# Kernel optimization log

Hardware: AMD Instinct MI355X
Metric: run time of the kernel (lower is better)

Reference implementation:

```python
import jax, jax.numpy as jnp
import numpy as np

B, T, C, H = 4, 2048, 1024, 16


def setup_inputs() -> dict:
    key = jax.random.key(0)
    ks = jax.random.split(key, 8)
    s = 0.02
    return {
        "xq": jax.random.normal(ks[0], (B, T, C), jnp.float32),
        "xk": jax.random.normal(ks[1], (B, T, C), jnp.float32),
        "xv": jax.random.normal(ks[2], (B, T, C), jnp.float32),
        "Wq": jax.random.normal(ks[3], (C, C), jnp.float32) * s,
        "Wk": jax.random.normal(ks[4], (C, C), jnp.float32) * s,
        "Wv": jax.random.normal(ks[5], (C, C), jnp.float32) * s,
        "Wo": jax.random.normal(ks[6], (C, C), jnp.float32) * s,
        "bo": jnp.zeros((C,), jnp.float32),
    }


def reference(xq, xk, xv, Wq, Wk, Wv, Wo, bo):
    # torch nn.Linear: y = x @ W.T
    q = xq @ Wq.T  # (B,T,C)
    k = xk @ Wk.T
    v = xv @ Wv.T
    hd = C // H
    # (B,T,C) -> (B,H,T,hd)
    q = q.reshape(B, T, H, hd).transpose(0, 2, 1, 3)
    k = k.reshape(B, T, H, hd).transpose(0, 2, 1, 3)
    v = v.reshape(B, T, H, hd).transpose(0, 2, 1, 3)
    scale = 1.0 / jnp.sqrt(jnp.asarray(hd, q.dtype))
    att = jnp.einsum("bhqd,bhkd->bhqk", q, k) * scale  # (B,H,T,T)
    causal = jnp.tril(jnp.ones((T, T), bool))
    att = jnp.where(causal, att, jnp.asarray(-jnp.inf, att.dtype))
    att = jax.nn.softmax(att, axis=-1)
    y = jnp.einsum("bhqk,bhkd->bhqd", att, v)  # (B,H,T,hd)
    y = y.transpose(0, 2, 1, 3).reshape(B, T, C)
    return y @ Wo.T + bo
```

## Files before the change

kernel.cpp:

```cpp
#include <hip/hip_runtime.h>
#include <stdint.h>

#define B_ 4
#define T_ 2048
#define C_ 1024
#define H_ 16
#define HD 64

typedef __attribute__((ext_vector_type(8))) short bf16x8;
typedef __attribute__((ext_vector_type(4))) short bf16x4;
typedef __attribute__((ext_vector_type(4))) float v4f;
typedef __attribute__((ext_vector_type(4))) uint32_t v4u;

static __device__ __forceinline__ short f2bf(float f) {
    union { float f; uint32_t u; } v; v.f = f;
    uint32_t u = v.u;
    uint32_t r = (u + 0x7fffu + ((u >> 16) & 1u)) >> 16;
    return (short)(r & 0xffffu);
}
static __device__ __forceinline__ uint32_t pack2(float x, float y) {
    uint32_t a = __float_as_uint(x) + 0x8000u;
    uint32_t b = __float_as_uint(y) + 0x8000u;
    return __builtin_amdgcn_perm(b, a, 0x07060302u);
}
static __device__ __forceinline__ uint32_t pack2t(float x, float y) {
    return __builtin_amdgcn_perm(__float_as_uint(y), __float_as_uint(x), 0x07060302u);
}
static __device__ __forceinline__ void gload_lds16(const void* g, void* l) {
    __builtin_amdgcn_global_load_lds(
        (const __attribute__((address_space(1))) void*)g,
        (__attribute__((address_space(3))) void*)l, 16, 0, 0);
}

__global__ __launch_bounds__(256) void convx(
    const float* __restrict__ x0, const float* __restrict__ x1,
    short* __restrict__ o0, short* __restrict__ o1,
    const float* __restrict__ w0, const float* __restrict__ w1,
    const float* __restrict__ w2, const float* __restrict__ w3,
    short* __restrict__ wout)
{
    int bid = blockIdx.x;
    const float* src; short* dst; size_t id;
    if (bid < 8192) {
        src = (bid < 4096) ? x0 : x1;
        dst = (bid < 4096) ? o0 : o1;
        id = (size_t)(bid & 4095) * 256 + threadIdx.x;
    } else {
        int wb = bid - 8192;
        int wi = wb >> 9;
        src = (wi == 0) ? w0 : (wi == 1) ? w1 : (wi == 2) ? w2 : w3;
        dst = wout + (size_t)wi * (C_ * C_);
        id = (size_t)(wb & 511) * 256 + threadIdx.x;
    }
    const float* p = src + id * 8;
    v4f a0 = *(const v4f*)p, a1 = *(const v4f*)(p + 4);
    v4u dv;
    dv[0] = pack2(a0[0], a0[1]); dv[1] = pack2(a0[2], a0[3]);
    dv[2] = pack2(a1[0], a1[1]); dv[3] = pack2(a1[2], a1[3]);
    *(v4u*)&dst[id * 8] = dv;
}


__global__ __launch_bounds__(256) void proj_gemm(
    const short* __restrict__ Xq, const short* __restrict__ Xk,
    const short* __restrict__ Wb, const float* __restrict__ xv,
    short* __restrict__ Qh, short* __restrict__ Kh, short* __restrict__ Vt,
    float qscale)
{
    const int K = 1024;
    __shared__ short As[128 * 64];
    __shared__ short Bs[128 * 64];
    const int t = threadIdx.x;
    const int w = t >> 6, l = t & 63, g = l >> 4, c = l & 15;
    const int wm = w & 1, wn = w >> 1;
    const int z = blockIdx.z;
    const int m0 = (z == 2 ? blockIdx.y : blockIdx.x) * 128;
    const int n0 = (z == 2 ? blockIdx.x : blockIdx.y) * 128;
    const short* Ab = (z == 0) ? Xq : (z == 1) ? Xk : (Wb + 2 * C_ * C_);
    const short* Bb = (z == 0) ? Wb : (Wb + C_ * C_);

    const int srow = l >> 3;
    const int sch = (l & 7) ^ (l >> 3);
    const int rch = c & 7;

    v4f acc[4][4];
#pragma unroll
    for (int i = 0; i < 4; ++i)
#pragma unroll
        for (int j = 0; j < 4; ++j) acc[i][j] = (v4f){0.f, 0.f, 0.f, 0.f};

    for (int k0 = 0; k0 < K; k0 += 64) {
        __syncthreads();
#pragma unroll
        for (int i = 0; i < 4; ++i) {
            int sp = w * 4 + i;
            gload_lds16(Ab + (size_t)(m0 + sp * 8 + srow) * K + k0 + sch * 8,
                        &As[sp * 512]);
        }
        if (z < 2) {
#pragma unroll
            for (int i = 0; i < 4; ++i) {
                int sp = w * 4 + i;
                gload_lds16(Bb + (size_t)(n0 + sp * 8 + srow) * K + k0 + sch * 8,
                            &Bs[sp * 512]);
            }
        } else {
#pragma unroll
            for (int i = 0; i < 4; ++i) {
                int id = i * 256 + t;
                int rr = id >> 3, cc = id & 7;
                const float* p = xv + (size_t)(n0 + rr) * K + k0 + cc * 8;
                v4f a0 = *(const v4f*)p, a1 = *(const v4f*)(p + 4);
                v4u dv;
                dv[0] = pack2(a0[0], a0[1]); dv[1] = pack2(a0[2], a0[3]);
                dv[2] = pack2(a1[0], a1[1]); dv[3] = pack2(a1[2], a1[3]);
                *(v4u*)&Bs[rr * 64 + ((cc ^ (rr & 7)) * 8)] = dv;
            }
        }
        __syncthreads();
#pragma unroll
        for (int s = 0; s < 2; ++s) {
            const int kch = ((4 * s + g) ^ rch) * 8;
            bf16x8 af[4], bfr[4];
#pragma unroll
            for (int i = 0; i < 4; ++i)
                af[i] = *(const bf16x8*)&As[(wm * 64 + i * 16 + c) * 64 + kch];
#pragma unroll
            for (int j = 0; j < 4; ++j)
                bfr[j] = *(const bf16x8*)&Bs[(wn * 64 + j * 16 + c) * 64 + kch];
#pragma unroll
            for (int i = 0; i < 4; ++i)
#pragma unroll
                for (int j = 0; j < 4; ++j)
                    acc[i][j] = __builtin_amdgcn_mfma_f32_16x16x32_bf16(af[i], bfr[j], acc[i][j], 0, 0, 0);
        }
    }
    if (z < 2) {
        short* Out = (z == 0) ? Qh : Kh;
        const float os = (z == 0) ? qscale : 1.0f;
#pragma unroll
        for (int i = 0; i < 4; ++i)
#pragma unroll
            for (int j = 0; j < 4; ++j)
#pragma unroll
                for (int r = 0; r < 4; ++r) {
                    int m = m0 + wm * 64 + i * 16 + g * 4 + r;
                    int n = n0 + wn * 64 + j * 16 + c;
                    int b = m >> 11, tt = m & (T_ - 1);
                    int h = n >> 6, d = n & 63;
                    Out[((size_t)(b * H_ + h) * T_ + tt) * HD + d] = f2bf(acc[i][j][r] * os);
                }
    } else {
#pragma unroll
        for (int i = 0; i < 4; ++i)
#pragma unroll
            for (int j = 0; j < 4; ++j)
#pragma unroll
                for (int r = 0; r < 4; ++r) {
                    int m = m0 + wm * 64 + i * 16 + g * 4 + r;
                    int n = n0 + wn * 64 + j * 16 + c;
                    int b = n >> 11, tt = n & (T_ - 1);
                    int h = m >> 6, d = m & 63;
                    Vt[((size_t)(b * H_ + h) * HD + d) * T_ + tt] = f2bf(acc[i][j][r]);
                }
    }
}

__global__ __launch_bounds__(256) void gemm_o(
    const short* __restrict__ Yb, const short* __restrict__ Wo,
    float* __restrict__ Out, const float* __restrict__ bias)
{
    const int K = 1024;
    __shared__ short As[128 * 64];
    __shared__ short Bs[128 * 64];
    const int t = threadIdx.x;
    const int w = t >> 6, l = t & 63, g = l >> 4, c = l & 15;
    const int wm = w & 1, wn = w >> 1;
    const int m0 = blockIdx.x * 128, n0 = blockIdx.y * 128;

    const int srow = l >> 3;
    const int sch = (l & 7) ^ (l >> 3);
    const int rch = c & 7;

    v4f acc[4][4];
#pragma unroll
    for (int i = 0; i < 4; ++i)
#pragma unroll
        for (int j = 0; j < 4; ++j) acc[i][j] = (v4f){0.f, 0.f, 0.f, 0.f};

    for (int k0 = 0; k0 < K; k0 += 64) {
        __syncthreads();
#pragma unroll
        for (int i = 0; i < 4; ++i) {
            int sp = w * 4 + i;
            gload_lds16(Yb + (size_t)(m0 + sp * 8 + srow) * K + k0 + sch * 8,
                        &As[sp * 512]);
            gload_lds16(Wo + (size_t)(n0 + sp * 8 + srow) * K + k0 + sch * 8,
                        &Bs[sp * 512]);
        }
        __syncthreads();
#pragma unroll
        for (int s = 0; s < 2; ++s) {
            const int kch = ((4 * s + g) ^ rch) * 8;
            bf16x8 af[4], bfr[4];
#pragma unroll
            for (int i = 0; i < 4; ++i)
                af[i] = *(const bf16x8*)&As[(wm * 64 + i * 16 + c) * 64 + kch];
#pragma unroll
            for (int j = 0; j < 4; ++j)
                bfr[j] = *(const bf16x8*)&Bs[(wn * 64 + j * 16 + c) * 64 + kch];
#pragma unroll
            for (int i = 0; i < 4; ++i)
#pragma unroll
                for (int j = 0; j < 4; ++j)
                    acc[i][j] = __builtin_amdgcn_mfma_f32_16x16x32_bf16(af[i], bfr[j], acc[i][j], 0, 0, 0);
        }
    }
#pragma unroll
    for (int i = 0; i < 4; ++i)
#pragma unroll
        for (int j = 0; j < 4; ++j)
#pragma unroll
            for (int r = 0; r < 4; ++r) {
                int m = m0 + wm * 64 + i * 16 + g * 4 + r;
                int n = n0 + wn * 64 + j * 16 + c;
                Out[(size_t)m * C_ + n] = acc[i][j][r] + bias[n];
            }
}

__global__ __launch_bounds__(256) void attn_kernel(
    const short* __restrict__ Q, const short* __restrict__ Kp,
    const short* __restrict__ Vt, short* __restrict__ Y)
{
    __shared__ short Ks[2 * 64 * 32];
    __shared__ short Vs[64 * 72];
    const int t = threadIdx.x;
    const int w = t >> 6, l = t & 63, g = l >> 4, c = l & 15;
    const int bid = blockIdx.x;
    const int slot = bid >> 3;
    const int p = slot & 15;
    const size_t bh = (size_t)((bid & 7) * 8 + (slot >> 4));

    const int srow = l >> 2;
    const int sch = (l & 3) ^ ((l >> 3) & 3);
    const int gs = (g ^ ((c >> 1) & 3)) * 8;

    bf16x8 ones;
#pragma unroll
    for (int i = 0; i < 8; ++i) ones[i] = (short)0x3F80;

    for (int qi = 0; qi < 2; ++qi) {
        const int qt = qi ? (31 - p) : p;
        const int qbase = qt * 64;

        bf16x8 qf0, qf1;
        {
            const short* qp = &Q[(bh * T_ + qbase + w * 16 + c) * HD + g * 8];
            qf0 = *(const bf16x8*)qp;
            qf1 = *(const bf16x8*)(qp + 32);
        }

        v4f O[4], accl;
        accl = (v4f){0.f, 0.f, 0.f, 0.f};
#pragma unroll
        for (int d = 0; d < 4; ++d) O[d] = (v4f){0.f, 0.f, 0.f, 0.f};

        for (int kb = 0; kb <= qt; ++kb) {
            const int kbase = kb * 64;
            __syncthreads();
#pragma unroll
            for (int i = 0; i < 2; ++i) {
                int gi = w * 2 + i;
                int hk = gi >> 2, rb = gi & 3;
                const short* gp = &Kp[(bh * T_ + kbase + rb * 16 + srow) * HD + hk * 32 + sch * 8];
                gload_lds16(gp, &Ks[hk * 2048 + rb * 512]);
            }
#pragma unroll
            for (int i = 0; i < 2; ++i) {
                int id = i * 256 + t;
                int rr = id >> 3, cc = id & 7;
                *(bf16x8*)&Vs[rr * 72 + cc * 8] =
                    *(const bf16x8*)&Vt[(bh * HD + rr) * T_ + kbase + cc * 8];
            }
            __syncthreads();

            float s2[4][4];
#pragma unroll
            for (int j = 0; j < 4; ++j) {
                bf16x8 kf0 = *(const bf16x8*)&Ks[(j * 16 + c) * 32 + gs];
                bf16x8 kf1 = *(const bf16x8*)&Ks[2048 + (j * 16 + c) * 32 + gs];
                v4f sa = (v4f){0.f, 0.f, 0.f, 0.f};
                sa = __builtin_amdgcn_mfma_f32_16x16x32_bf16(kf0, qf0, sa, 0, 0, 0);
                sa = __builtin_amdgcn_mfma_f32_16x16x32_bf16(kf1, qf1, sa, 0, 0, 0);
#pragma unroll
                for (int r = 0; r < 4; ++r) s2[j][r] = sa[r];
            }
            if (kb == qt) {
                const int q = qbase + w * 16 + c;
#pragma unroll
                for (int j = 0; j < 4; ++j)
#pragma unroll
                    for (int r = 0; r < 4; ++r) {
                        int key = kbase + j * 16 + g * 4 + r;
                        if (key > q) s2[j][r] = -3.0e38f;
                    }
            }
            union { bf16x8 v; uint32_t u[4]; } pa[2];
#pragma unroll
            for (int s = 0; s < 2; ++s)
#pragma unroll
                for (int wi = 0; wi < 4; ++wi) {
                    int j = 2 * s + (wi >> 1);
                    int r0 = (wi & 1) * 2;
                    float x = __builtin_amdgcn_exp2f(s2[j][r0]);
                    float y = __builtin_amdgcn_exp2f(s2[j][r0 + 1]);
                    pa[s].u[wi] = pack2t(x, y);
                }
#pragma unroll
            for (int s = 0; s < 2; ++s) {
                bf16x8 af = pa[s].v;
#pragma unroll
                for (int d = 0; d < 4; ++d) {
                    const short* vp = &Vs[(d * 16 + c) * 72 + s * 32 + g * 4];
                    union { bf16x8 v8; bf16x4 v4[2]; } vu;
                    vu.v4[0] = *(const bf16x4*)vp;
                    vu.v4[1] = *(const bf16x4*)(vp + 16);
                    O[d] = __builtin_amdgcn_mfma_f32_16x16x32_bf16(af, vu.v8, O[d], 0, 0, 0);
                }
                accl = __builtin_amdgcn_mfma_f32_16x16x32_bf16(af, ones, accl, 0, 0, 0);
            }
        }
#pragma unroll
        for (int r = 0; r < 4; ++r) {
            float rl = 1.0f / accl[r];
            size_t rowoff = ((size_t)(bh >> 4) * T_ + qbase + w * 16 + g * 4 + r) * C_ + (bh & 15) * HD;
#pragma unroll
            for (int d = 0; d < 4; ++d)
                Y[rowoff + d * 16 + c] = f2bf(O[d][r] * rl);
        }
    }
}

extern "C" void kernel_launch(void* const* d_in, const int* in_sizes, int n_in,
                              void* d_out, int out_size, void* d_ws, size_t ws_size,
                              hipStream_t stream) {
    const float* xq = (const float*)d_in[0];
    const float* xk = (const float*)d_in[1];
    const float* xv = (const float*)d_in[2];
    const float* Wq = (const float*)d_in[3];
    const float* Wk = (const float*)d_in[4];
    const float* Wv = (const float*)d_in[5];
    const float* Wo = (const float*)d_in[6];
    const float* bo = (const float*)d_in[7];

    const size_t NE = (size_t)B_ * H_ * T_ * HD;
    const size_t WE = (size_t)C_ * C_;
    short* Qh    = (short*)d_ws;
    short* Kh    = Qh + NE;
    short* slotA = Kh + NE;
    short* slotB = slotA + NE;
    short* Wbf   = slotB + NE;
    short* Vt    = (short*)d_out;

    const float qscale = 0.18033688011112042f;
    dim3 blk(256);

    hipLaunchKernelGGL(convx, dim3(10240), blk, 0, stream,
                       xq, xk, slotA, slotB, Wq, Wk, Wv, Wo, Wbf);
    hipLaunchKernelGGL(proj_gemm, dim3(64, 8, 3), blk, 0, stream,
                       slotA, slotB, Wbf, xv, Qh, Kh, Vt, qscale);
    hipLaunchKernelGGL(attn_kernel, dim3(B_ * H_ * (T_ / 128)), blk, 0, stream,
                       Qh, Kh, Vt, slotA);
    hipLaunchKernelGGL(gemm_o, dim3(64, 8), blk, 0, stream,
                       slotA, Wbf + 3 * WE, (float*)d_out, bo);
}
```

Measured before the change: 307.1 us.

## Fuse paired causal query tiles into one KV sweep sharing K/V loads

```diff
diff --git a/kernel.cpp b/kernel.cpp
--- a/kernel.cpp
+++ b/kernel.cpp
@@ -249,54 +249,70 @@
 #pragma unroll
     for (int i = 0; i < 8; ++i) ones[i] = (short)0x3F80;
 
-    for (int qi = 0; qi < 2; ++qi) {
-        const int qt = qi ? (31 - p) : p;
-        const int qbase = qt * 64;
-
-        bf16x8 qf0, qf1;
+    const int qtL = p, qtH = 31 - p;
+    const int qbL = qtL * 64, qbH = qtH * 64;
+
+    bf16x8 qL0, qL1, qH0, qH1;
+    {
+        const short* qp = &Q[(bh * T_ + qbL + w * 16 + c) * HD + g * 8];
+        qL0 = *(const bf16x8*)qp;
+        qL1 = *(const bf16x8*)(qp + 32);
+    }
+    {
+        const short* qp = &Q[(bh * T_ + qbH + w * 16 + c) * HD + g * 8];
+        qH0 = *(const bf16x8*)qp;
+        qH1 = *(const bf16x8*)(qp + 32);
+    }
+
+    v4f OL[4], OH[4], accL, accH;
+    accL = (v4f){0.f, 0.f, 0.f, 0.f};
+    accH = (v4f){0.f, 0.f, 0.f, 0.f};
+#pragma unroll
+    for (int d = 0; d < 4; ++d) {
+        OL[d] = (v4f){0.f, 0.f, 0.f, 0.f};
+        OH[d] = (v4f){0.f, 0.f, 0.f, 0.f};
+    }
+
+    for (int kb = 0; kb <= qtH; ++kb) {
+        const int kbase = kb * 64;
+        __syncthreads();
+#pragma unroll
+        for (int i = 0; i < 2; ++i) {
+            int gi = w * 2 + i;
+            int hk = gi >> 2, rb = gi & 3;
+            const short* gp = &Kp[(bh * T_ + kbase + rb * 16 + srow) * HD + hk * 32 + sch * 8];
+            gload_lds16(gp, &Ks[hk * 2048 + rb * 512]);
+        }
+#pragma unroll
+        for (int i = 0; i < 2; ++i) {
+            int id = i * 256 + t;
+            int rr = id >> 3, cc = id & 7;
+            *(bf16x8*)&Vs[rr * 72 + cc * 8] =
+                *(const bf16x8*)&Vt[(bh * HD + rr) * T_ + kbase + cc * 8];
+        }
+        __syncthreads();
+
+        bf16x8 kf0[4], kf1[4];
+#pragma unroll
+        for (int j = 0; j < 4; ++j) {
+            kf0[j] = *(const bf16x8*)&Ks[(j * 16 + c) * 32 + gs];
+            kf1[j] = *(const bf16x8*)&Ks[2048 + (j * 16 + c) * 32 + gs];
+        }
+
         {
-            const short* qp = &Q[(bh * T_ + qbase + w * 16 + c) * HD + g * 8];
-            qf0 = *(const bf16x8*)qp;
-            qf1 = *(const bf16x8*)(qp + 32);
-        }
-
-        v4f O[4], accl;
-        accl = (v4f){0.f, 0.f, 0.f, 0.f};
-#pragma unroll
-        for (int d = 0; d < 4; ++d) O[d] = (v4f){0.f, 0.f, 0.f, 0.f};
-
-        for (int kb = 0; kb <= qt; ++kb) {
-            const int kbase = kb * 64;
-            __syncthreads();
-#pragma unroll
-            for (int i = 0; i < 2; ++i) {
-                int gi = w * 2 + i;
-                int hk = gi >> 2, rb = gi & 3;
-                const short* gp = &Kp[(bh * T_ + kbase + rb * 16 + srow) * HD + hk * 32 + sch * 8];
-                gload_lds16(gp, &Ks[hk * 2048 + rb * 512]);
-            }
-#pragma unroll
-            for (int i = 0; i < 2; ++i) {
-                int id = i * 256 + t;
-                int rr = id >> 3, cc = id & 7;
-                *(bf16x8*)&Vs[rr * 72 + cc * 8] =
-                    *(const bf16x8*)&Vt[(bh * HD + rr) * T_ + kbase + cc * 8];
-            }
-            __syncthreads();
-
             float s2[4][4];
+            __builtin_amdgcn_s_setprio(1);
 #pragma unroll
             for (int j = 0; j < 4; ++j) {
-                bf16x8 kf0 = *(const bf16x8*)&Ks[(j * 16 + c) * 32 + gs];
-                bf16x8 kf1 = *(const bf16x8*)&Ks[2048 + (j * 16 + c) * 32 + gs];
                 v4f sa = (v4f){0.f, 0.f, 0.f, 0.f};
-                sa = __builtin_amdgcn_mfma_f32_16x16x32_bf16(kf0, qf0, sa, 0, 0, 0);
-                sa = __builtin_amdgcn_mfma_f32_16x16x32_bf16(kf1, qf1, sa, 0, 0, 0);
+                sa = __builtin_amdgcn_mfma_f32_16x16x32_bf16(kf0[j], qH0, sa, 0, 0, 0);
+                sa = __builtin_amdgcn_mfma_f32_16x16x32_bf16(kf1[j], qH1, sa, 0, 0, 0);
 #pragma unroll
                 for (int r = 0; r < 4; ++r) s2[j][r] = sa[r];
             }
-            if (kb == qt) {
-                const int q = qbase + w * 16 + c;
+            __builtin_amdgcn_s_setprio(0);
+            if (kb == qtH) {
+                const int q = qbH + w * 16 + c;
 #pragma unroll
                 for (int j = 0; j < 4; ++j)
 #pragma unroll
@@ -316,6 +332,7 @@
                     float y = __builtin_amdgcn_exp2f(s2[j][r0 + 1]);
                     pa[s].u[wi] = pack2t(x, y);
                 }
+            __builtin_amdgcn_s_setprio(1);
 #pragma unroll
             for (int s = 0; s < 2; ++s) {
                 bf16x8 af = pa[s].v;
@@ -325,18 +342,74 @@
                     union { bf16x8 v8; bf16x4 v4[2]; } vu;
                     vu.v4[0] = *(const bf16x4*)vp;
                     vu.v4[1] = *(const bf16x4*)(vp + 16);
-                    O[d] = __builtin_amdgcn_mfma_f32_16x16x32_bf16(af, vu.v8, O[d], 0, 0, 0);
-                }
-                accl = __builtin_amdgcn_mfma_f32_16x16x32_bf16(af, ones, accl, 0, 0, 0);
-            }
-        }
-#pragma unroll
-        for (int r = 0; r < 4; ++r) {
-            float rl = 1.0f / accl[r];
-            size_t rowoff = ((size_t)(bh >> 4) * T_ + qbase + w * 16 + g * 4 + r) * C_ + (bh & 15) * HD;
-#pragma unroll
-            for (int d = 0; d < 4; ++d)
-                Y[rowoff + d * 16 + c] = f2bf(O[d][r] * rl);
+                    OH[d] = __builtin_amdgcn_mfma_f32_16x16x32_bf16(af, vu.v8, OH[d], 0, 0, 0);
+                }
+                accH = __builtin_amdgcn_mfma_f32_16x16x32_bf16(af, ones, accH, 0, 0, 0);
+            }
+            __builtin_amdgcn_s_setprio(0);
+        }
+
+        if (kb <= qtL) {
+            float s2[4][4];
+            __builtin_amdgcn_s_setprio(1);
+#pragma unroll
+            for (int j = 0; j < 4; ++j) {
+                v4f sa = (v4f){0.f, 0.f, 0.f, 0.f};
+                sa = __builtin_amdgcn_mfma_f32_16x16x32_bf16(kf0[j], qL0, sa, 0, 0, 0);
+                sa = __builtin_amdgcn_mfma_f32_16x16x32_bf16(kf1[j], qL1, sa, 0, 0, 0);
+#pragma unroll
+                for (int r = 0; r < 4; ++r) s2[j][r] = sa[r];
+            }
+            __builtin_amdgcn_s_setprio(0);
+            if (kb == qtL) {
+                const int q = qbL + w * 16 + c;
+#pragma unroll
+                for (int j = 0; j < 4; ++j)
+#pragma unroll
+                    for (int r = 0; r < 4; ++r) {
+                        int key = kbase + j * 16 + g * 4 + r;
+                        if (key > q) s2[j][r] = -3.0e38f;
+                    }
+            }
+            union { bf16x8 v; uint32_t u[4]; } pa[2];
+#pragma unroll
+            for (int s = 0; s < 2; ++s)
+#pragma unroll
+                for (int wi = 0; wi < 4; ++wi) {
+                    int j = 2 * s + (wi >> 1);
+                    int r0 = (wi & 1) * 2;
+                    float x = __builtin_amdgcn_exp2f(s2[j][r0]);
+                    float y = __builtin_amdgcn_exp2f(s2[j][r0 + 1]);
+                    pa[s].u[wi] = pack2t(x, y);
+                }
+            __builtin_amdgcn_s_setprio(1);
+#pragma unroll
+            for (int s = 0; s < 2; ++s) {
+                bf16x8 af = pa[s].v;
+#pragma unroll
+                for (int d = 0; d < 4; ++d) {
+                    const short* vp = &Vs[(d * 16 + c) * 72 + s * 32 + g * 4];
+                    union { bf16x8 v8; bf16x4 v4[2]; } vu;
+                    vu.v4[0] = *(const bf16x4*)vp;
+                    vu.v4[1] = *(const bf16x4*)(vp + 16);
+                    OL[d] = __builtin_amdgcn_mfma_f32_16x16x32_bf16(af, vu.v8, OL[d], 0, 0, 0);
+                }
+                accL = __builtin_amdgcn_mfma_f32_16x16x32_bf16(af, ones, accL, 0, 0, 0);
+            }
+            __builtin_amdgcn_s_setprio(0);
+        }
+    }
+#pragma unroll
+    for (int r = 0; r < 4; ++r) {
+        float rlL = 1.0f / accL[r];
+        float rlH = 1.0f / accH[r];
+        size_t baseoff = ((size_t)(bh >> 4) * T_ + w * 16 + g * 4 + r) * C_ + (bh & 15) * HD;
+        size_t offL = baseoff + (size_t)qbL * C_;
+        size_t offH = baseoff + (size_t)qbH * C_;
+#pragma unroll
+        for (int d = 0; d < 4; ++d) {
+            Y[offL + d * 16 + c] = f2bf(OL[d][r] * rlL);
+            Y[offH + d * 16 + c] = f2bf(OH[d][r] * rlH);
         }
     }
 }
```

New measurement: 316.3 us. 3.0% more time.
